# Optimization experiments

Hardware: AMD Instinct MI355X
Metric: run time of the kernel (lower is better)

## Reference

```python
import jax, jax.numpy as jnp
import numpy as np

T, N, D, E = 4, 50000, 32, 800000
V_TH = 1.0      # v_threshold
ALPHA = 4.0     # surrogate-gradient sharpness


def setup_inputs() -> dict:
    key = jax.random.key(0)
    k1, k2, k3, k4 = jax.random.split(key, 4)
    s_seq = jax.random.normal(k1, (T, N, D), dtype=jnp.float32) * 0.5
    z_seq = jax.random.normal(k2, (N, D), dtype=jnp.float32) * 0.5
    edge_index = jax.random.randint(k3, (2, E), 0, N, dtype=jnp.int64)
    # GCNConv weight (bias=False), Glorot-ish scale
    W = jax.random.normal(k4, (D, D), dtype=jnp.float32) / np.sqrt(D).astype(np.float32)
    return {"s_seq": s_seq, "z_seq": z_seq, "W": W, "edge_index": edge_index}


def _gcn_conv(x, W, edge_index, n_nodes):
    """PyG GCNConv with add_self_loops=True, normalize=True, bias=False.
    x: [T,N,D]; returns [T,N,D]."""
    src, dst = edge_index[0], edge_index[1]
    ones = jnp.ones(src.shape[0], dtype=x.dtype)
    deg = jax.ops.segment_sum(ones, dst, num_segments=n_nodes) + 1.0  # +1 self loop
    dinv = jax.lax.rsqrt(deg)                                        # [N]
    xw = jnp.einsum('tnd,df->tnf', x, W)                             # dense transform
    norm = dinv[src] * dinv[dst]                                     # [E]
    msgs = xw[:, src, :] * norm[None, :, None]                       # [T,E,D] gather
    agg = jax.vmap(lambda m: jax.ops.segment_sum(m, dst, num_segments=n_nodes))(msgs)
    # self-loop contribution with norm dinv[i]^2
    return agg + xw * (dinv * dinv)[None, :, None]


def _spike(v):
    # Heaviside spike with surrogate (sigmoid) gradient, straight-through.
    s = (v >= V_TH).astype(v.dtype)
    sg = jax.nn.sigmoid(ALPHA * (v - V_TH))
    return s + sg - jax.lax.stop_gradient(sg)


def reference(s_seq, z_seq, W, edge_index):
    n_nodes = s_seq.shape[1]
    x_seq = _gcn_conv(s_seq, W, edge_index, n_nodes)   # [T,N,D]  (dropout p=0.0 is identity)
    y_seq = x_seq.mean(0)                              # temporal mean [N,D]
    # Riemannian IF node: integrate-and-fire over time with soft reset;
    # latent state z drifts by the temporal mean (Euclidean proxy for expmap).
    def step(v, x_t):
        v = v + x_t
        o = _spike(v)
        v = v - o * V_TH
        return v, o
    v0 = jnp.zeros_like(z_seq)
    _, o_seq = jax.lax.scan(step, v0, x_seq)           # [T,N,D]
    z_new = z_seq + y_seq
    return o_seq, z_new
```

## Files before the change

### kernel.cpp

```cpp
#include <hip/hip_runtime.h>
#include <hip/hip_fp16.h>

#define TSTEPS 4
#define DIM 32
#define BINW_SHIFT 8
#define NB 256
#define HB 128
#define GROWS 128
#define SP_CH 2048
#define CAPB 4608
#define PAD_PER_BIN 772

__device__ __forceinline__ float4 ldx4h(const __half* p) {
    uint2 u = *(const uint2*)p;
    __half2 h0 = *(__half2*)&u.x;
    __half2 h1 = *(__half2*)&u.y;
    float2 a = __half22float2(h0);
    float2 b = __half22float2(h1);
    return make_float4(a.x, a.y, b.x, b.y);
}

__global__ __launch_bounds__(256) void histxw_kernel(
    const int* __restrict__ ei, int* __restrict__ ghistPB, int* __restrict__ cursor,
    const float* __restrict__ s, const float* __restrict__ W, __half* __restrict__ xwp,
    int E, int rows, int N, int hch) {
    __shared__ float4 sW4[32][8];
    __shared__ float sS[GROWS][36];
    __shared__ int lh[NB];
    int tid = threadIdx.x;
    if ((int)blockIdx.x < HB) {
        lh[tid] = 0;
        __syncthreads();
        int beg = blockIdx.x * hch;
        int end = min(beg + hch, E);
        for (int e = beg + tid; e < end; e += 256)
            atomicAdd(&lh[ei[E + e] >> BINW_SHIFT], 1);
        __syncthreads();
        ghistPB[blockIdx.x * NB + tid] = lh[tid];
        if (blockIdx.x == 0) cursor[tid] = 0;
        return;
    }
    int row = tid >> 3;
    int cg = tid & 7;
    sW4[row >> 0][cg] = ((const float4*)W)[tid];
    int rowBase = (blockIdx.x - HB) * GROWS;
#pragma unroll
    for (int j = 0; j < 4; j++) {
        int r = rowBase + row + j * 32;
        float4 sv = (r < rows) ? ((const float4*)s)[(size_t)r * 8 + cg]
                               : make_float4(0.f, 0.f, 0.f, 0.f);
        *(float4*)&sS[row + j * 32][cg * 4] = sv;
    }
    __syncthreads();
    float4 a0 = make_float4(0.f, 0.f, 0.f, 0.f);
    float4 a1 = a0, a2 = a0, a3 = a0;
#pragma unroll
    for (int k = 0; k < 32; k++) {
        float4 wv = sW4[k][cg];
        float s0 = sS[row][k];
        float s1 = sS[row + 32][k];
        float s2 = sS[row + 64][k];
        float s3 = sS[row + 96][k];
        a0.x += s0 * wv.x; a0.y += s0 * wv.y; a0.z += s0 * wv.z; a0.w += s0 * wv.w;
        a1.x += s1 * wv.x; a1.y += s1 * wv.y; a1.z += s1 * wv.z; a1.w += s1 * wv.w;
        a2.x += s2 * wv.x; a2.y += s2 * wv.y; a2.z += s2 * wv.z; a2.w += s2 * wv.w;
        a3.x += s3 * wv.x; a3.y += s3 * wv.y; a3.z += s3 * wv.z; a3.w += s3 * wv.w;
    }
    float4 accs[4] = {a0, a1, a2, a3};
#pragma unroll
    for (int j = 0; j < 4; j++) {
        int r = rowBase + row + j * 32;
        if (r < rows) {
            int t = r / N;
            int n = r - t * N;
            __half2 h0 = __floats2half2_rn(accs[j].x, accs[j].y);
            __half2 h1 = __floats2half2_rn(accs[j].z, accs[j].w);
            uint2 u;
            u.x = *(unsigned int*)&h0;
            u.y = *(unsigned int*)&h1;
            *(uint2*)(xwp + (size_t)n * 128 + t * 32 + cg * 4) = u;
        }
    }
}

__global__ __launch_bounds__(256) void split_kernel(
    const int* __restrict__ ei, const int* __restrict__ ghistPB,
    int* __restrict__ cursor, int2* __restrict__ esorted, int E) {
    __shared__ int phw[4][NB];
    __shared__ int sBS[NB], pscan[NB], gb[NB], pcur[NB];
    __shared__ int2 sbuf[SP_CH];
    int tid = threadIdx.x;
    int gv = 0;
    for (int r = 0; r < HB; r++) gv += ghistPB[r * NB + tid];
    sBS[tid] = gv;
    __syncthreads();
    for (int off = 1; off < 256; off <<= 1) {
        int t = (tid >= off) ? sBS[tid - off] : 0;
        __syncthreads();
        sBS[tid] += t;
        __syncthreads();
    }
    int binStart = sBS[tid] - gv;
    phw[0][tid] = 0; phw[1][tid] = 0; phw[2][tid] = 0; phw[3][tid] = 0;
    __syncthreads();
    int beg = blockIdx.x * SP_CH;
    int end = min(beg + SP_CH, E);
    int cnt = end - beg;
    int wv = tid >> 6;
    for (int e = beg + tid; e < end; e += 256)
        atomicAdd(&phw[wv][ei[E + e] >> BINW_SHIFT], 1);
    __syncthreads();
    int v = phw[0][tid] + phw[1][tid] + phw[2][tid] + phw[3][tid];
    pscan[tid] = v;
    __syncthreads();
    for (int off = 1; off < 256; off <<= 1) {
        int t = (tid >= off) ? pscan[tid - off] : 0;
        __syncthreads();
        pscan[tid] += t;
        __syncthreads();
    }
    pscan[tid] -= v;
    pcur[tid] = pscan[tid];
    gb[tid] = v ? (binStart + atomicAdd(&cursor[tid], v)) : 0;
    __syncthreads();
    for (int e = beg + tid; e < end; e += 256) {
        int2 r;
        r.x = ei[e];
        r.y = ei[E + e];
        int b = r.y >> BINW_SHIFT;
        int p = atomicAdd(&pcur[b], 1);
        sbuf[p] = r;
    }
    __syncthreads();
    for (int idx = tid; idx < cnt; idx += 256) {
        int2 e = sbuf[idx];
        int b = e.y >> BINW_SHIFT;
        esorted[gb[b] + (idx - pscan[b])] = e;
    }
}

__global__ __launch_bounds__(256) void csr_kernel(
    const int* __restrict__ ghistPB, const int2* __restrict__ esorted,
    int* __restrict__ rec, int* __restrict__ offs, int* __restrict__ deg,
    float* __restrict__ dinv, int N) {
    __shared__ int sorted[CAPB + 768];
    __shared__ int sc[NB], lh[NB], loff[NB], lcur[NB];
    __shared__ int s_ebeg, s_cnt;
    int bin = blockIdx.x;
    int tid = threadIdx.x;
    int gv = 0;
    for (int r = 0; r < HB; r++) gv += ghistPB[r * NB + tid];
    sc[tid] = gv;
    __syncthreads();
    for (int off = 1; off < 256; off <<= 1) {
        int t = (tid >= off) ? sc[tid - off] : 0;
        __syncthreads();
        sc[tid] += t;
        __syncthreads();
    }
    if (tid == bin) { s_ebeg = sc[tid] - gv; s_cnt = gv; }
    __syncthreads();
    int ebeg = s_ebeg;
    int cnt = min(s_cnt, CAPB);
    int gbase = ((ebeg + 3) & ~3) + PAD_PER_BIN * bin;
    lh[tid] = 0;
    __syncthreads();
    for (int i = tid; i < cnt; i += 256)
        atomicAdd(&lh[esorted[ebeg + i].y & 255], 1);
    __syncthreads();
    int padded = (lh[tid] + 3) & ~3;
    sc[tid] = padded;
    __syncthreads();
    for (int off = 1; off < 256; off <<= 1) {
        int t = (tid >= off) ? sc[tid - off] : 0;
        __syncthreads();
        sc[tid] += t;
        __syncthreads();
    }
    loff[tid] = sc[tid] - padded;
    lcur[tid] = 0;
    __syncthreads();
    int run = sc[255];
    for (int i = tid; i < run; i += 256) sorted[i] = 0;
    __syncthreads();
    for (int i = tid; i < cnt; i += 256) {
        int2 e = esorted[ebeg + i];
        int ln = e.y & 255;
        int p = atomicAdd(&lcur[ln], 1);
        sorted[loff[ln] + p] = e.x;
    }
    __syncthreads();
    for (int i = tid; i < run; i += 256) rec[gbase + i] = sorted[i];
    int n = (bin << BINW_SHIFT) + tid;
    if (n < N) {
        offs[n] = gbase + loff[tid];
        deg[n] = lh[tid];
        dinv[n] = rsqrtf((float)lh[tid] + 1.0f);
    }
}

__global__ __launch_bounds__(256) void gather_kernel(
    const int* __restrict__ rec, const int* __restrict__ offs,
    const int* __restrict__ deg, const __half* __restrict__ xwp,
    const float* __restrict__ dinv, const float* __restrict__ z,
    float* __restrict__ out, int N) {
    int gid = blockIdx.x * 256 + threadIdx.x;
    int n = gid >> 5;
    if (n >= N) return;
    int wl = threadIdx.x & 63;
    int half_ = wl >> 5;
    int l = wl & 31;
    int q = l & 7;
    long lofs = l * 4;

    float dn = dinv[n];
    int beg = offs[n];
    int cntn = deg[n];

    float4 acc = make_float4(0.f, 0.f, 0.f, 0.f);
    int i = 0;
    for (; i + 8 <= cntn; i += 8) {
        int4 sa = *(const int4*)(rec + beg + i);
        int4 sb = *(const int4*)(rec + beg + i + 4);
        float n0 = dinv[sa.x] * dn, n1 = dinv[sa.y] * dn;
        float n2 = dinv[sa.z] * dn, n3 = dinv[sa.w] * dn;
        float n4 = dinv[sb.x] * dn, n5 = dinv[sb.y] * dn;
        float n6 = dinv[sb.z] * dn, n7 = dinv[sb.w] * dn;
        float4 p0 = ldx4h(xwp + (long)sa.x * 128 + lofs);
        float4 p1 = ldx4h(xwp + (long)sa.y * 128 + lofs);
        float4 p2 = ldx4h(xwp + (long)sa.z * 128 + lofs);
        float4 p3 = ldx4h(xwp + (long)sa.w * 128 + lofs);
        float4 p4 = ldx4h(xwp + (long)sb.x * 128 + lofs);
        float4 p5 = ldx4h(xwp + (long)sb.y * 128 + lofs);
        float4 p6 = ldx4h(xwp + (long)sb.z * 128 + lofs);
        float4 p7 = ldx4h(xwp + (long)sb.w * 128 + lofs);
        acc.x += n0 * p0.x + n1 * p1.x + n2 * p2.x + n3 * p3.x
               + n4 * p4.x + n5 * p5.x + n6 * p6.x + n7 * p7.x;
        acc.y += n0 * p0.y + n1 * p1.y + n2 * p2.y + n3 * p3.y
               + n4 * p4.y + n5 * p5.y + n6 * p6.y + n7 * p7.y;
        acc.z += n0 * p0.z + n1 * p1.z + n2 * p2.z + n3 * p3.z
               + n4 * p4.z + n5 * p5.z + n6 * p6.z + n7 * p7.z;
        acc.w += n0 * p0.w + n1 * p1.w + n2 * p2.w + n3 * p3.w
               + n4 * p4.w + n5 * p5.w + n6 * p6.w + n7 * p7.w;
    }
    for (; i < cntn; i += 4) {
        int4 s4 = *(const int4*)(rec + beg + i);
        int rem = cntn - i;
        int i0 = s4.x;
        int i1 = (rem > 1) ? s4.y : i0;
        int i2 = (rem > 2) ? s4.z : i0;
        int i3 = (rem > 3) ? s4.w : i0;
        float n0 = dinv[i0] * dn;
        float n1 = (rem > 1) ? dinv[i1] * dn : 0.f;
        float n2 = (rem > 2) ? dinv[i2] * dn : 0.f;
        float n3 = (rem > 3) ? dinv[i3] * dn : 0.f;
        float4 p0 = ldx4h(xwp + (long)i0 * 128 + lofs);
        float4 p1 = ldx4h(xwp + (long)i1 * 128 + lofs);
        float4 p2 = ldx4h(xwp + (long)i2 * 128 + lofs);
        float4 p3 = ldx4h(xwp + (long)i3 * 128 + lofs);
        acc.x += n0 * p0.x + n1 * p1.x + n2 * p2.x + n3 * p3.x;
        acc.y += n0 * p0.y + n1 * p1.y + n2 * p2.y + n3 * p3.y;
        acc.z += n0 * p0.z + n1 * p1.z + n2 * p2.z + n3 * p3.z;
        acc.w += n0 * p0.w + n1 * p1.w + n2 * p2.w + n3 * p3.w;
    }
    {
        float d2 = dn * dn;
        float4 ps = ldx4h(xwp + (long)n * 128 + lofs);
        acc.x += d2 * ps.x;
        acc.y += d2 * ps.y;
        acc.z += d2 * ps.z;
        acc.w += d2 * ps.w;
    }
    float4 xs[TSTEPS];
#pragma unroll
    for (int t = 0; t < TSTEPS; t++) {
        int srcLane = half_ * 32 + t * 8 + q;
        xs[t].x = __shfl(acc.x, srcLane, 64);
        xs[t].y = __shfl(acc.y, srcLane, 64);
        xs[t].z = __shfl(acc.z, srcLane, 64);
        xs[t].w = __shfl(acc.w, srcLane, 64);
    }
    if (l < 8) {
        float4 y;
        y.x = (xs[0].x + xs[1].x + xs[2].x + xs[3].x) * 0.25f;
        y.y = (xs[0].y + xs[1].y + xs[2].y + xs[3].y) * 0.25f;
        y.z = (xs[0].z + xs[1].z + xs[2].z + xs[3].z) * 0.25f;
        y.w = (xs[0].w + xs[1].w + xs[2].w + xs[3].w) * 0.25f;
        float4 v = make_float4(0.f, 0.f, 0.f, 0.f);
        int colBase = n * 32 + q * 4;
#pragma unroll
        for (int t = 0; t < TSTEPS; t++) {
            float4 o;
            v.x += xs[t].x; o.x = (v.x >= 1.0f) ? 1.0f : 0.0f; v.x -= o.x;
            v.y += xs[t].y; o.y = (v.y >= 1.0f) ? 1.0f : 0.0f; v.y -= o.y;
            v.z += xs[t].z; o.z = (v.z >= 1.0f) ? 1.0f : 0.0f; v.z -= o.z;
            v.w += xs[t].w; o.w = (v.w >= 1.0f) ? 1.0f : 0.0f; v.w -= o.w;
            *(float4*)(out + (size_t)t * N * 32 + colBase) = o;
        }
        float4 zv = *(const float4*)(z + colBase);
        float4 zn;
        zn.x = zv.x + y.x;
        zn.y = zv.y + y.y;
        zn.z = zv.z + y.z;
        zn.w = zv.w + y.w;
        *(float4*)(out + (size_t)TSTEPS * N * 32 + colBase) = zn;
    }
}

extern "C" void kernel_launch(void* const* d_in, const int* in_sizes, int n_in,
                              void* d_out, int out_size, void* d_ws, size_t ws_size,
                              hipStream_t stream) {
    const float* s_seq = (const float*)d_in[0];
    const float* z_seq = (const float*)d_in[1];
    const float* W     = (const float*)d_in[2];
    const int*   ei    = (const int*)d_in[3];
    float* out = (float*)d_out;

    int N = in_sizes[1] / DIM;
    int E = in_sizes[3] / 2;
    int rows = TSTEPS * N;
    int nb = (N + 255) >> BINW_SHIFT;
    int nchunks = (E + SP_CH - 1) / SP_CH;

    char* w = (char*)d_ws;
    __half* xwp     = (__half*)w; w += (size_t)rows * DIM * 2;
    int2*  esorted  = (int2*)w;   w += (size_t)E * 8;
    int*   rec      = (int*)w;    w += ((size_t)E + PAD_PER_BIN * nb + 16) * 4;
    int*   offs     = (int*)w;    w += (size_t)N * 4;
    int*   deg      = (int*)w;    w += (size_t)N * 4;
    float* dinv     = (float*)w;  w += (size_t)N * 4;
    int*   ghistPB  = (int*)w;    w += (size_t)HB * NB * 4;
    int*   cursor   = (int*)w;    w += NB * 4;

    int hch = (E + HB - 1) / HB;
    int xwBlocks = (rows + GROWS - 1) / GROWS;
    histxw_kernel<<<HB + xwBlocks, 256, 0, stream>>>(ei, ghistPB, cursor, s_seq, W,
                                                     xwp, E, rows, N, hch);
    split_kernel<<<nchunks, 256, 0, stream>>>(ei, ghistPB, cursor, esorted, E);
    csr_kernel<<<nb, 256, 0, stream>>>(ghistPB, esorted, rec, offs, deg, dinv, N);
    gather_kernel<<<(N * 32 + 255) / 256, 256, 0, stream>>>(rec, offs, deg, xwp,
                                                            dinv, z_seq, out, N);
}
```

Measured before the change: 181.3 us.

## Pack edges into 32-bit keys, move GEMM into split kernel, simplify CSR build

The dense xW transform moves out of the histogram kernel and into the split kernel's grid, so the histogram launch is small and the GEMM runs alongside the edge split. Sorted edges are packed into one 32-bit word (16-bit source, destination in the high bits), which halves esorted traffic. The split kernel publishes the bin prefix scan so the CSR kernel no longer re-reduces the per-block histograms. The CSR kernel now scatters straight to global memory instead of staging through LDS, and the per-bin capacity clamp is removed. Packing assumes node ids fit in 16 bits (N=50000 does), and the padding slots in rec are no longer zeroed.

```diff
diff --git a/kernel.cpp b/kernel.cpp
--- a/kernel.cpp
+++ b/kernel.cpp
@@ -8,7 +8,6 @@
 #define HB 128
 #define GROWS 128
 #define SP_CH 2048
-#define CAPB 4608
 #define PAD_PER_BIN 772
 
 __device__ __forceinline__ float4 ldx4h(const __half* p) {
@@ -20,76 +19,85 @@
     return make_float4(a.x, a.y, b.x, b.y);
 }
 
-__global__ __launch_bounds__(256) void histxw_kernel(
+__global__ __launch_bounds__(256) void hist_kernel(
     const int* __restrict__ ei, int* __restrict__ ghistPB, int* __restrict__ cursor,
-    const float* __restrict__ s, const float* __restrict__ W, __half* __restrict__ xwp,
-    int E, int rows, int N, int hch) {
-    __shared__ float4 sW4[32][8];
-    __shared__ float sS[GROWS][36];
+    int E, int hch) {
     __shared__ int lh[NB];
     int tid = threadIdx.x;
-    if ((int)blockIdx.x < HB) {
-        lh[tid] = 0;
-        __syncthreads();
-        int beg = blockIdx.x * hch;
-        int end = min(beg + hch, E);
-        for (int e = beg + tid; e < end; e += 256)
-            atomicAdd(&lh[ei[E + e] >> BINW_SHIFT], 1);
-        __syncthreads();
-        ghistPB[blockIdx.x * NB + tid] = lh[tid];
-        if (blockIdx.x == 0) cursor[tid] = 0;
+    lh[tid] = 0;
+    __syncthreads();
+    int beg = blockIdx.x * hch;
+    int end = min(beg + hch, E);
+    for (int e = beg + tid; e < end; e += 256)
+        atomicAdd(&lh[ei[E + e] >> BINW_SHIFT], 1);
+    __syncthreads();
+    ghistPB[blockIdx.x * NB + tid] = lh[tid];
+    if (blockIdx.x == 0) cursor[tid] = 0;
+}
+
+__global__ __launch_bounds__(256) void splitgemm_kernel(
+    const int* __restrict__ ei, const int* __restrict__ ghistPB,
+    int* __restrict__ cursor, unsigned int* __restrict__ esorted,
+    int* __restrict__ binScan,
+    const float* __restrict__ s, const float* __restrict__ W,
+    __half* __restrict__ xwp, int E, int rows, int N, int nchunks) {
+    __shared__ __align__(16) char smem[22528];
+    int tid = threadIdx.x;
+
+    if ((int)blockIdx.x >= nchunks) {
+        float4 (*sW4)[8] = (float4 (*)[8])smem;
+        float  (*sS)[36] = (float (*)[36])(smem + 4096);
+        int row = tid >> 3;
+        int cg  = tid & 7;
+        sW4[row][cg] = ((const float4*)W)[tid];
+        int rowBase = ((int)blockIdx.x - nchunks) * GROWS;
+#pragma unroll
+        for (int j = 0; j < 4; j++) {
+            int r = rowBase + row + j * 32;
+            float4 sv = (r < rows) ? ((const float4*)s)[(size_t)r * 8 + cg]
+                                   : make_float4(0.f, 0.f, 0.f, 0.f);
+            *(float4*)&sS[row + j * 32][cg * 4] = sv;
+        }
+        __syncthreads();
+        float4 a0 = make_float4(0.f, 0.f, 0.f, 0.f);
+        float4 a1 = a0, a2 = a0, a3 = a0;
+#pragma unroll
+        for (int k = 0; k < 32; k++) {
+            float4 wv = sW4[k][cg];
+            float s0 = sS[row][k];
+            float s1 = sS[row + 32][k];
+            float s2 = sS[row + 64][k];
+            float s3 = sS[row + 96][k];
+            a0.x += s0 * wv.x; a0.y += s0 * wv.y; a0.z += s0 * wv.z; a0.w += s0 * wv.w;
+            a1.x += s1 * wv.x; a1.y += s1 * wv.y; a1.z += s1 * wv.z; a1.w += s1 * wv.w;
+            a2.x += s2 * wv.x; a2.y += s2 * wv.y; a2.z += s2 * wv.z; a2.w += s2 * wv.w;
+            a3.x += s3 * wv.x; a3.y += s3 * wv.y; a3.z += s3 * wv.z; a3.w += s3 * wv.w;
+        }
+        float4 accs[4] = {a0, a1, a2, a3};
+#pragma unroll
+        for (int j = 0; j < 4; j++) {
+            int r = rowBase + row + j * 32;
+            if (r < rows) {
+                int t = r / N;
+                int n = r - t * N;
+                __half2 h0 = __floats2half2_rn(accs[j].x, accs[j].y);
+                __half2 h1 = __floats2half2_rn(accs[j].z, accs[j].w);
+                uint2 u;
+                u.x = *(unsigned int*)&h0;
+                u.y = *(unsigned int*)&h1;
+                *(uint2*)(xwp + (size_t)n * 128 + t * 32 + cg * 4) = u;
+            }
+        }
         return;
     }
-    int row = tid >> 3;
-    int cg = tid & 7;
-    sW4[row >> 0][cg] = ((const float4*)W)[tid];
-    int rowBase = (blockIdx.x - HB) * GROWS;
-#pragma unroll
-    for (int j = 0; j < 4; j++) {
-        int r = rowBase + row + j * 32;
-        float4 sv = (r < rows) ? ((const float4*)s)[(size_t)r * 8 + cg]
-                               : make_float4(0.f, 0.f, 0.f, 0.f);
-        *(float4*)&sS[row + j * 32][cg * 4] = sv;
-    }
-    __syncthreads();
-    float4 a0 = make_float4(0.f, 0.f, 0.f, 0.f);
-    float4 a1 = a0, a2 = a0, a3 = a0;
-#pragma unroll
-    for (int k = 0; k < 32; k++) {
-        float4 wv = sW4[k][cg];
-        float s0 = sS[row][k];
-        float s1 = sS[row + 32][k];
-        float s2 = sS[row + 64][k];
-        float s3 = sS[row + 96][k];
-        a0.x += s0 * wv.x; a0.y += s0 * wv.y; a0.z += s0 * wv.z; a0.w += s0 * wv.w;
-        a1.x += s1 * wv.x; a1.y += s1 * wv.y; a1.z += s1 * wv.z; a1.w += s1 * wv.w;
-        a2.x += s2 * wv.x; a2.y += s2 * wv.y; a2.z += s2 * wv.z; a2.w += s2 * wv.w;
-        a3.x += s3 * wv.x; a3.y += s3 * wv.y; a3.z += s3 * wv.z; a3.w += s3 * wv.w;
-    }
-    float4 accs[4] = {a0, a1, a2, a3};
-#pragma unroll
-    for (int j = 0; j < 4; j++) {
-        int r = rowBase + row + j * 32;
-        if (r < rows) {
-            int t = r / N;
-            int n = r - t * N;
-            __half2 h0 = __floats2half2_rn(accs[j].x, accs[j].y);
-            __half2 h1 = __floats2half2_rn(accs[j].z, accs[j].w);
-            uint2 u;
-            u.x = *(unsigned int*)&h0;
-            u.y = *(unsigned int*)&h1;
-            *(uint2*)(xwp + (size_t)n * 128 + t * 32 + cg * 4) = u;
-        }
-    }
-}
-
-__global__ __launch_bounds__(256) void split_kernel(
-    const int* __restrict__ ei, const int* __restrict__ ghistPB,
-    int* __restrict__ cursor, int2* __restrict__ esorted, int E) {
-    __shared__ int phw[4][NB];
-    __shared__ int sBS[NB], pscan[NB], gb[NB], pcur[NB];
-    __shared__ int2 sbuf[SP_CH];
-    int tid = threadIdx.x;
+
+    int* phw   = (int*)smem;
+    int* sBS   = (int*)(smem + 4096);
+    int* pscan = (int*)(smem + 5120);
+    int* gb    = (int*)(smem + 6144);
+    int* pcur  = (int*)(smem + 7168);
+    unsigned int* sbuf = (unsigned int*)(smem + 8192);
+
     int gv = 0;
     for (int r = 0; r < HB; r++) gv += ghistPB[r * NB + tid];
     sBS[tid] = gv;
@@ -101,16 +109,18 @@
         __syncthreads();
     }
     int binStart = sBS[tid] - gv;
-    phw[0][tid] = 0; phw[1][tid] = 0; phw[2][tid] = 0; phw[3][tid] = 0;
+    if (blockIdx.x == 0) binScan[tid] = sBS[tid];
+    phw[0 * NB + tid] = 0; phw[1 * NB + tid] = 0;
+    phw[2 * NB + tid] = 0; phw[3 * NB + tid] = 0;
     __syncthreads();
     int beg = blockIdx.x * SP_CH;
     int end = min(beg + SP_CH, E);
     int cnt = end - beg;
     int wv = tid >> 6;
     for (int e = beg + tid; e < end; e += 256)
-        atomicAdd(&phw[wv][ei[E + e] >> BINW_SHIFT], 1);
-    __syncthreads();
-    int v = phw[0][tid] + phw[1][tid] + phw[2][tid] + phw[3][tid];
+        atomicAdd(&phw[wv * NB + (ei[E + e] >> BINW_SHIFT)], 1);
+    __syncthreads();
+    int v = phw[0 * NB + tid] + phw[1 * NB + tid] + phw[2 * NB + tid] + phw[3 * NB + tid];
     pscan[tid] = v;
     __syncthreads();
     for (int off = 1; off < 256; off <<= 1) {
@@ -124,33 +134,45 @@
     gb[tid] = v ? (binStart + atomicAdd(&cursor[tid], v)) : 0;
     __syncthreads();
     for (int e = beg + tid; e < end; e += 256) {
-        int2 r;
-        r.x = ei[e];
-        r.y = ei[E + e];
-        int b = r.y >> BINW_SHIFT;
+        int sx = ei[e];
+        int dx = ei[E + e];
+        unsigned int pk = (unsigned int)sx | ((unsigned int)dx << 16);
+        int b = dx >> BINW_SHIFT;
         int p = atomicAdd(&pcur[b], 1);
-        sbuf[p] = r;
+        sbuf[p] = pk;
     }
     __syncthreads();
     for (int idx = tid; idx < cnt; idx += 256) {
-        int2 e = sbuf[idx];
-        int b = e.y >> BINW_SHIFT;
+        unsigned int e = sbuf[idx];
+        int b = e >> 24;
         esorted[gb[b] + (idx - pscan[b])] = e;
     }
 }
 
 __global__ __launch_bounds__(256) void csr_kernel(
-    const int* __restrict__ ghistPB, const int2* __restrict__ esorted,
+    const int* __restrict__ binScan, const unsigned int* __restrict__ esorted,
     int* __restrict__ rec, int* __restrict__ offs, int* __restrict__ deg,
     float* __restrict__ dinv, int N) {
-    __shared__ int sorted[CAPB + 768];
-    __shared__ int sc[NB], lh[NB], loff[NB], lcur[NB];
+    __shared__ int lh[NB], sc[NB], loff[NB], lcur[NB];
     __shared__ int s_ebeg, s_cnt;
     int bin = blockIdx.x;
     int tid = threadIdx.x;
-    int gv = 0;
-    for (int r = 0; r < HB; r++) gv += ghistPB[r * NB + tid];
-    sc[tid] = gv;
+    if (tid == 0) {
+        int e0 = bin ? binScan[bin - 1] : 0;
+        int e1 = binScan[bin];
+        s_ebeg = e0;
+        s_cnt = e1 - e0;
+    }
+    lh[tid] = 0;
+    __syncthreads();
+    int ebeg = s_ebeg;
+    int cnt = s_cnt;
+    int gbase = ((ebeg + 3) & ~3) + PAD_PER_BIN * bin;
+    for (int i = tid; i < cnt; i += 256)
+        atomicAdd(&lh[(esorted[ebeg + i] >> 16) & 255], 1);
+    __syncthreads();
+    int padded = (lh[tid] + 3) & ~3;
+    sc[tid] = padded;
     __syncthreads();
     for (int off = 1; off < 256; off <<= 1) {
         int t = (tid >= off) ? sc[tid - off] : 0;
@@ -158,39 +180,15 @@
         sc[tid] += t;
         __syncthreads();
     }
-    if (tid == bin) { s_ebeg = sc[tid] - gv; s_cnt = gv; }
-    __syncthreads();
-    int ebeg = s_ebeg;
-    int cnt = min(s_cnt, CAPB);
-    int gbase = ((ebeg + 3) & ~3) + PAD_PER_BIN * bin;
-    lh[tid] = 0;
-    __syncthreads();
-    for (int i = tid; i < cnt; i += 256)
-        atomicAdd(&lh[esorted[ebeg + i].y & 255], 1);
-    __syncthreads();
-    int padded = (lh[tid] + 3) & ~3;
-    sc[tid] = padded;
-    __syncthreads();
-    for (int off = 1; off < 256; off <<= 1) {
-        int t = (tid >= off) ? sc[tid - off] : 0;
-        __syncthreads();
-        sc[tid] += t;
-        __syncthreads();
-    }
     loff[tid] = sc[tid] - padded;
     lcur[tid] = 0;
     __syncthreads();
-    int run = sc[255];
-    for (int i = tid; i < run; i += 256) sorted[i] = 0;
-    __syncthreads();
     for (int i = tid; i < cnt; i += 256) {
-        int2 e = esorted[ebeg + i];
-        int ln = e.y & 255;
+        unsigned int e = esorted[ebeg + i];
+        int ln = (e >> 16) & 255;
         int p = atomicAdd(&lcur[ln], 1);
-        sorted[loff[ln] + p] = e.x;
-    }
-    __syncthreads();
-    for (int i = tid; i < run; i += 256) rec[gbase + i] = sorted[i];
+        rec[gbase + loff[ln] + p] = (int)(e & 0xFFFFu);
+    }
     int n = (bin << BINW_SHIFT) + tid;
     if (n < N) {
         offs[n] = gbase + loff[tid];
@@ -323,21 +321,22 @@
     int nchunks = (E + SP_CH - 1) / SP_CH;
 
     char* w = (char*)d_ws;
-    __half* xwp     = (__half*)w; w += (size_t)rows * DIM * 2;
-    int2*  esorted  = (int2*)w;   w += (size_t)E * 8;
+    __half* xwp          = (__half*)w;       w += (size_t)rows * DIM * 2;
+    unsigned int* esorted = (unsigned int*)w; w += (size_t)E * 4;
     int*   rec      = (int*)w;    w += ((size_t)E + PAD_PER_BIN * nb + 16) * 4;
     int*   offs     = (int*)w;    w += (size_t)N * 4;
     int*   deg      = (int*)w;    w += (size_t)N * 4;
     float* dinv     = (float*)w;  w += (size_t)N * 4;
     int*   ghistPB  = (int*)w;    w += (size_t)HB * NB * 4;
     int*   cursor   = (int*)w;    w += NB * 4;
+    int*   binScan  = (int*)w;    w += NB * 4;
 
     int hch = (E + HB - 1) / HB;
     int xwBlocks = (rows + GROWS - 1) / GROWS;
-    histxw_kernel<<<HB + xwBlocks, 256, 0, stream>>>(ei, ghistPB, cursor, s_seq, W,
-                                                     xwp, E, rows, N, hch);
-    split_kernel<<<nchunks, 256, 0, stream>>>(ei, ghistPB, cursor, esorted, E);
-    csr_kernel<<<nb, 256, 0, stream>>>(ghistPB, esorted, rec, offs, deg, dinv, N);
+    hist_kernel<<<HB, 256, 0, stream>>>(ei, ghistPB, cursor, E, hch);
+    splitgemm_kernel<<<nchunks + xwBlocks, 256, 0, stream>>>(
+        ei, ghistPB, cursor, esorted, binScan, s_seq, W, xwp, E, rows, N, nchunks);
+    csr_kernel<<<nb, 256, 0, stream>>>(binScan, esorted, rec, offs, deg, dinv, N);
     gather_kernel<<<(N * 32 + 255) / 256, 256, 0, stream>>>(rec, offs, deg, xwp,
                                                             dinv, z_seq, out, N);
 }
```

Measured after the change: 181.7 us. No clear change (+0.2%).
